# Optimization experiments

Hardware: AMD Instinct MI355X
Metric: run time of the kernel (lower is better)

Reference implementation:

```python
import jax, jax.numpy as jnp
import numpy as np
from jax import lax

B, CIN, COUT, H, W = 16, 320, 320, 64, 64
R, NUM_LORAS, LORA_STRIDE, SCALE, K = 4, 50, 4, 1.0, 3


def setup_inputs() -> dict:
    key = jax.random.key(0)
    k1, k2, k3, k4, k5, k6 = jax.random.split(key, 6)
    x = jax.random.normal(k1, (B, CIN, H, W), dtype=jnp.float32)
    lora_id = jax.random.randint(k2, (B,), 0, NUM_LORAS * LORA_STRIDE, dtype=jnp.int64)
    conv_w = jax.random.normal(k3, (COUT, CIN, K, K), dtype=jnp.float32) * (1.0 / np.sqrt(CIN * K * K))
    conv_b = jax.random.normal(k4, (COUT,), dtype=jnp.float32) * 0.01
    # stacked LoRA banks: down [L, r, Cin, 3, 3], up [L, Cout, r] (1x1 conv squeezed)
    down_w = jax.random.normal(k5, (NUM_LORAS, R, CIN, K, K), dtype=jnp.float32) * (1.0 / R)
    up_w = jax.random.normal(k6, (NUM_LORAS, COUT, R), dtype=jnp.float32) * 0.02
    return {"x": x, "conv_w": conv_w, "conv_b": conv_b, "down_w": down_w, "up_w": up_w, "lora_id": lora_id}


def _conv3x3(x, w):
    # x: [N, C, H, W], w: [O, C, 3, 3], stride 1, padding 1
    return lax.conv_general_dilated(x, w, (1, 1), [(1, 1), (1, 1)],
                                    dimension_numbers=("NCHW", "OIHW", "NCHW"))


def reference(x, conv_w, conv_b, down_w, up_w, lora_id):
    idx = lora_id // LORA_STRIDE                      # [B]
    active = (idx >= 0).astype(x.dtype)               # [B] mask; negative -> base conv only
    safe = jnp.clip(idx, 0, NUM_LORAS - 1)
    # base conv on full batch (dropout is identity at inference)
    base = _conv3x3(x, conv_w) + conv_b[None, :, None, None]  # [B, Cout, H, W]
    # per-sample gathered down conv (3x3), vmapped over batch (MoE-style dispatch)
    wd = down_w[safe]                                 # [B, r, Cin, 3, 3]
    down = jax.vmap(lambda xi, wi: _conv3x3(xi[None], wi)[0])(x, wd)  # [B, r, H, W]
    # per-sample 1x1 up conv as einsum with gathered up weights
    up = jnp.einsum("brhw,bor->bohw", down, up_w[safe])  # [B, Cout, H, W]
    return base + SCALE * up * active[:, None, None, None]
```

## Files before the change

### kernel.cpp

```cpp
#include <hip/hip_runtime.h>

typedef unsigned short ushort_t;
typedef unsigned int   uint_t;
typedef __attribute__((ext_vector_type(8))) short  short8;
typedef __attribute__((ext_vector_type(4))) float  float4v;
typedef __attribute__((ext_vector_type(4))) uint_t uint4v;
typedef __attribute__((ext_vector_type(2))) uint_t uint2v;

#define B_    16
#define CIN_  320
#define COUT_ 320
#define NLORA 50
#define R_    4
#define NCH   10

#define XCHUNK (66*66*32)
#define WCHUNK (9*COUT_*32)
#define XPAD_ELEMS ((size_t)B_ * NCH * XCHUNK)
#define WEFF_OFF   (XPAD_ELEMS * 2)

__device__ __forceinline__ ushort_t bf16rne(float f) {
  uint_t u = __float_as_uint(f);
  u = (u + 0x7FFFu + ((u >> 16) & 1u)) >> 16;
  return (ushort_t)u;
}

__device__ __forceinline__ void gld16(const ushort_t* g, ushort_t* l) {
  __builtin_amdgcn_global_load_lds(
      (const __attribute__((address_space(1))) void*)g,
      (__attribute__((address_space(3))) void*)l,
      16, 0, 0);
}

__global__ __launch_bounds__(256)
void pad_convert(const float* __restrict__ x, ushort_t* __restrict__ x_pad) {
  __shared__ float t[64][65];
  const int cc  = blockIdx.x;
  const int h   = blockIdx.y;
  const int b   = blockIdx.z;
  const int tid = threadIdx.x;
  #pragma unroll
  for (int it = 0; it < 4; ++it) {
    int idx = it * 256 + tid;
    int cl = idx >> 4, w4 = (idx & 15) * 4;
    float4v v = *(const float4v*)(x +
        (((size_t)(b * CIN_ + cc * 64 + cl)) * 64 + h) * 64 + w4);
    t[cl][w4] = v[0]; t[cl][w4 + 1] = v[1];
    t[cl][w4 + 2] = v[2]; t[cl][w4 + 3] = v[3];
  }
  __syncthreads();
  #pragma unroll
  for (int it = 0; it < 4; ++it) {
    int j  = it * 256 + tid;
    int cq = j & 15, wl = j >> 4;
    int cl = cq * 4;
    uint_t u0 = (uint_t)bf16rne(t[cl][wl])     | ((uint_t)bf16rne(t[cl + 1][wl]) << 16);
    uint_t u1 = (uint_t)bf16rne(t[cl + 2][wl]) | ((uint_t)bf16rne(t[cl + 3][wl]) << 16);
    int chunk = cc * 2 + (cl >> 5);
    uint2v u; u[0] = u0; u[1] = u1;
    *(uint2v*)(x_pad + (((size_t)(b * NCH + chunk) * 66 + (h + 1)) * 66 + (wl + 1)) * 32
               + (cl & 31)) = u;
  }
  if (h == 0) {
    #pragma unroll
    for (int s = 0; s < 2; ++s) {
      ushort_t* base = x_pad + (size_t)(b * NCH + cc * 2 + s) * XCHUNK;
      for (int g = tid; g < 528; g += 256) {
        int r = (g >= 264) ? 1 : 0;
        int g2 = g - r * 264;
        int col = g2 >> 2, qg = g2 & 3;
        *(uint4v*)(base + ((size_t)(r * 65) * 66 + col) * 32 + qg * 8) = (uint4v)0u;
      }
      for (int g = tid; g < 512; g += 256) {
        int row = 1 + (g >> 3);
        int col = ((g >> 2) & 1) * 65;
        int qg  = g & 3;
        *(uint4v*)(base + ((size_t)row * 66 + col) * 32 + qg * 8) = (uint4v)0u;
      }
    }
  }
}

__global__ __launch_bounds__(320)
void merge_weights(const float* __restrict__ conv_w, const float* __restrict__ down_w,
                   const float* __restrict__ up_w,  const void* __restrict__ lora,
                   ushort_t* __restrict__ W_eff) {
  const int o = blockIdx.x;
  const int b = blockIdx.y;
  const int tid = threadIdx.x;

  const int* p32 = (const int*)lora;
  bool odd0 = true;
  #pragma unroll
  for (int i = 1; i < 16; i += 2) odd0 = odd0 && (p32[i] == 0);
  long long raw = odd0 ? ((const long long*)lora)[b] : (long long)p32[b];
  long long idx = (raw >= 0) ? (raw >> 2) : -(((-raw) + 3) >> 2);
  float act = (idx >= 0) ? 1.0f : 0.0f;
  int l = (int)(idx < 0 ? 0 : (idx > (NLORA - 1) ? (NLORA - 1) : idx));

  float up[R_];
  #pragma unroll
  for (int r = 0; r < R_; ++r)
    up[r] = up_w[((size_t)l * COUT_ + o) * R_ + r] * act;

  const float* cw = conv_w + (size_t)o * (CIN_ * 9);
  const float* dw = down_w + (size_t)l * (R_ * CIN_ * 9);
  #pragma unroll
  for (int it = 0; it < 9; ++it) {
    int j = it * 320 + tid;
    float v = cw[j] + up[0] * dw[j] + up[1] * dw[2880 + j]
                    + up[2] * dw[5760 + j] + up[3] * dw[8640 + j];
    int c   = j / 9;
    int tap = j - c * 9;
    W_eff[(((size_t)(b * NCH + (c >> 5)) * 9 + tap) * COUT_ + o) * 32 + (c & 31)]
        = bf16rne(v);
  }
}

#define XG    1360
#define XGP   1408
#define WG    1152
#define TOTG  2560
#define BUF_B (TOTG * 16)

__global__ __launch_bounds__(512, 4)
void conv_main(const ushort_t* __restrict__ x_pad, const ushort_t* __restrict__ W_eff,
               const float* __restrict__ conv_b, float* __restrict__ out) {
  __shared__ __align__(16) char smem[2 * BUF_B];

  const int tid = threadIdx.x;
  const int lin = blockIdx.x;
  const int wg  = (lin & 7) * 320 + (lin >> 3);
  const int b   = wg / 160;
  const int rem = wg - b * 160;
  const int o0  = (rem >> 4) * 32;
  const int hw  = rem & 15;
  const int h0  = (hw & 7) * 8;
  const int w0  = (hw >> 3) * 32;

  const int wv = tid >> 6;
  const int la = tid & 15;
  const int q  = (tid >> 4) & 3;

  const ushort_t* psrc[5];
  int step[5];
  #pragma unroll
  for (int r = 0; r < 5; ++r) {
    int g = r * 512 + tid;
    if (g < XGP) {
      int gx = (g < XG) ? g : (XG - 1);
      int qq = gx & 3, t = gx >> 2;
      int hh = t / 34, ww = t - hh * 34;
      int sq = qq ^ ((ww >> 1) & 3);
      psrc[r] = x_pad + (size_t)b * NCH * XCHUNK
              + (((h0 + hh) * 66 + (w0 + ww)) * 32 + sq * 8);
      step[r] = XCHUNK;
    } else {
      int gw = g - XGP;
      int qq = gw & 3, t2 = gw >> 2;
      int o = t2 & 31, tap = t2 >> 5;
      int sq = qq ^ ((o >> 1) & 3);
      psrc[r] = W_eff + (size_t)b * NCH * WCHUNK
              + ((tap * COUT_ + o0 + o) * 32 + sq * 8);
      step[r] = WCHUNK;
    }
  }

  float4v acc[2][2];
  #pragma unroll
  for (int i = 0; i < 2; ++i)
    #pragma unroll
    for (int n = 0; n < 2; ++n) acc[i][n] = (float4v)0.0f;

  auto STAGE = [&](int sel) {
    ushort_t* bufb = (ushort_t*)(smem + sel * BUF_B);
    #pragma unroll
    for (int r = 0; r < 5; ++r) {
      gld16(psrc[r], bufb + (r * 512 + wv * 64) * 8);
      psrc[r] += step[r];
    }
  };

  STAGE(0);
  int cur = 0;
  for (int t = 0; t < NCH; ++t) {
    asm volatile("" ::: "memory");
    __builtin_amdgcn_s_barrier();
    asm volatile("" ::: "memory");
    if (t < NCH - 1) STAGE(cur ^ 1);
    __builtin_amdgcn_sched_barrier(0);
    if (t < NCH - 1) asm volatile("s_waitcnt vmcnt(5)" ::: "memory");
    else             asm volatile("s_waitcnt vmcnt(0)" ::: "memory");
    __builtin_amdgcn_sched_barrier(0);
    __builtin_amdgcn_s_barrier();
    asm volatile("" ::: "memory");

    const ushort_t* xb = (const ushort_t*)(smem + cur * BUF_B);
    const ushort_t* wb = xb + XGP * 8;
    #pragma unroll
    for (int tap = 0; tap < 9; ++tap) {
      const int kh = tap / 3, kw = tap - kh * 3;
      const int ob0 = la, ob1 = 16 + la;
      short8 bf0 = *(const short8*)(wb + ((tap * 32 + ob0) * 4 + (q ^ ((ob0 >> 1) & 3))) * 8);
      short8 bf1 = *(const short8*)(wb + ((tap * 32 + ob1) * 4 + (q ^ ((ob1 >> 1) & 3))) * 8);
      const int hh = wv + kh;
      #pragma unroll
      for (int i = 0; i < 2; ++i) {
        int ww = i * 16 + la + kw;
        short8 af = *(const short8*)(xb + ((hh * 34 + ww) * 4 + (q ^ ((ww >> 1) & 3))) * 8);
        acc[i][0] = __builtin_amdgcn_mfma_f32_16x16x32_bf16(af, bf0, acc[i][0], 0, 0, 0);
        acc[i][1] = __builtin_amdgcn_mfma_f32_16x16x32_bf16(af, bf1, acc[i][1], 0, 0, 0);
      }
    }
    cur ^= 1;
  }

  __syncthreads();
  float* lc = (float*)smem;
  #pragma unroll
  for (int n = 0; n < 2; ++n) {
    const int n_loc = n * 16 + la;
    #pragma unroll
    for (int i = 0; i < 2; ++i)
      *(float4v*)(lc + n_loc * 260 + wv * 32 + i * 16 + q * 4) = acc[i][n];
  }
  __syncthreads();
  const size_t ob = ((size_t)(b * COUT_ + o0)) * 4096 + h0 * 64 + w0;
  for (int f = tid; f < 32 * 64; f += 512) {
    int n_loc = f >> 6;
    int m4 = (f & 63) * 4;
    int row = m4 >> 5, col = m4 & 31;
    float4v v = *(const float4v*)(lc + n_loc * 260 + m4);
    v += conv_b[o0 + n_loc];
    *(float4v*)(out + ob + (size_t)n_loc * 4096 + row * 64 + col) = v;
  }
}

extern "C" void kernel_launch(void* const* d_in, const int* in_sizes, int n_in,
                              void* d_out, int out_size, void* d_ws, size_t ws_size,
                              hipStream_t stream) {
  const float* x      = (const float*)d_in[0];
  const float* conv_w = (const float*)d_in[1];
  const float* conv_b = (const float*)d_in[2];
  const float* down_w = (const float*)d_in[3];
  const float* up_w   = (const float*)d_in[4];
  const void*  lora   = d_in[5];
  float* out = (float*)d_out;

  ushort_t* x_pad = (ushort_t*)d_ws;
  ushort_t* W_eff = (ushort_t*)((char*)d_ws + WEFF_OFF);

  pad_convert  <<<dim3(5, 64, 16), 256, 0, stream>>>(x, x_pad);
  merge_weights<<<dim3(320, 16),   320, 0, stream>>>(conv_w, down_w, up_w, lora, W_eff);
  conv_main    <<<dim3(2560),      512, 0, stream>>>(x_pad, W_eff, conv_b, out);
}
```

Measured before the change: 303.2 us.

## Split LoRA into separate down-projection pass and fuse up-projection into conv epilogue

Stops merging the LoRA weights into a per-sample effective conv weight. The main conv now uses one shared bf16 base weight for all samples instead of per-batch W_eff. A separate small MFMA kernel computes the rank-4 down conv, and the up projection plus bias is applied in the conv epilogue, which writes directly from registers instead of staging through LDS. Shared weights improve cache reuse and avoid writing 16 copies of the merged weight, at the cost of two extra launches, a rank-16-padded down conv, and a different numeric path where the LoRA term is now computed in bf16 separately.

```diff
diff --git a/kernel.cpp b/kernel.cpp
--- a/kernel.cpp
+++ b/kernel.cpp
@@ -16,8 +16,11 @@
 
 #define XCHUNK (66*66*32)
 #define WCHUNK (9*COUT_*32)
-#define XPAD_ELEMS ((size_t)B_ * NCH * XCHUNK)
-#define WEFF_OFF   (XPAD_ELEMS * 2)
+#define DCHUNK (9*16*32)
+
+#define WB16_OFF  44605440ULL
+#define DWNE_OFF  46448640ULL
+#define DOWN_OFF  47923200ULL
 
 __device__ __forceinline__ ushort_t bf16rne(float f) {
   uint_t u = __float_as_uint(f);
@@ -30,6 +33,18 @@
       (const __attribute__((address_space(1))) void*)g,
       (__attribute__((address_space(3))) void*)l,
       16, 0, 0);
+}
+
+__device__ __forceinline__ void lora_idx(const void* lora, int b, int* l_out,
+                                         float* act_out) {
+  const int* p32 = (const int*)lora;
+  bool odd0 = true;
+  #pragma unroll
+  for (int i = 1; i < 16; i += 2) odd0 = odd0 && (p32[i] == 0);
+  long long raw = odd0 ? ((const long long*)lora)[b] : (long long)p32[b];
+  long long idx = (raw >= 0) ? (raw >> 2) : -(((-raw) + 3) >> 2);
+  *act_out = (idx >= 0) ? 1.0f : 0.0f;
+  *l_out = (int)(idx < 0 ? 0 : (idx > (NLORA - 1) ? (NLORA - 1) : idx));
 }
 
 __global__ __launch_bounds__(256)
@@ -81,39 +96,140 @@
   }
 }
 
-__global__ __launch_bounds__(320)
-void merge_weights(const float* __restrict__ conv_w, const float* __restrict__ down_w,
-                   const float* __restrict__ up_w,  const void* __restrict__ lora,
-                   ushort_t* __restrict__ W_eff) {
-  const int o = blockIdx.x;
-  const int b = blockIdx.y;
+__global__ __launch_bounds__(512)
+void wconv(const float* __restrict__ conv_w, ushort_t* __restrict__ wb16) {
+  int idx = blockIdx.x * 512 + threadIdx.x;
+  int c5 = idx & 31;
+  int o  = (idx >> 5) % COUT_;
+  int rest = idx / (COUT_ * 32);
+  int tap = rest % 9, chunk = rest / 9;
+  wb16[idx] = bf16rne(conv_w[((size_t)o * CIN_ + chunk * 32 + c5) * 9 + tap]);
+}
+
+__global__ __launch_bounds__(512)
+void dwnconv(const float* __restrict__ down_w, const void* __restrict__ lora,
+             ushort_t* __restrict__ dwn_eff) {
+  const int b = blockIdx.x;
+  int l; float act;
+  lora_idx(lora, b, &l, &act);
+  ushort_t* dst = dwn_eff + (size_t)b * (NCH * DCHUNK);
+  const float* src = down_w + (size_t)l * (R_ * CIN_ * 9);
+  for (int it = 0; it < 90; ++it) {
+    int idx = it * 512 + threadIdx.x;
+    int c5 = idx & 31;
+    int r  = (idx >> 5) & 15;
+    int rest = idx >> 9;
+    int tap = rest % 9, chunk = rest / 9;
+    float v = (r < R_) ? act * src[((size_t)(r * CIN_) + chunk * 32 + c5) * 9 + tap]
+                       : 0.0f;
+    dst[idx] = bf16rne(v);
+  }
+}
+
+#define LXG    1360
+#define LXGP   1408
+#define LWG    576
+#define LTOTG  2048
+#define LBUF_B (LTOTG * 16)
+
+__global__ __launch_bounds__(512)
+void lora_down(const ushort_t* __restrict__ x_pad, const ushort_t* __restrict__ dwn_eff,
+               float* __restrict__ down) {
+  __shared__ __align__(16) char smem[2 * LBUF_B];
+
   const int tid = threadIdx.x;
-
-  const int* p32 = (const int*)lora;
-  bool odd0 = true;
-  #pragma unroll
-  for (int i = 1; i < 16; i += 2) odd0 = odd0 && (p32[i] == 0);
-  long long raw = odd0 ? ((const long long*)lora)[b] : (long long)p32[b];
-  long long idx = (raw >= 0) ? (raw >> 2) : -(((-raw) + 3) >> 2);
-  float act = (idx >= 0) ? 1.0f : 0.0f;
-  int l = (int)(idx < 0 ? 0 : (idx > (NLORA - 1) ? (NLORA - 1) : idx));
-
-  float up[R_];
-  #pragma unroll
-  for (int r = 0; r < R_; ++r)
-    up[r] = up_w[((size_t)l * COUT_ + o) * R_ + r] * act;
-
-  const float* cw = conv_w + (size_t)o * (CIN_ * 9);
-  const float* dw = down_w + (size_t)l * (R_ * CIN_ * 9);
-  #pragma unroll
-  for (int it = 0; it < 9; ++it) {
-    int j = it * 320 + tid;
-    float v = cw[j] + up[0] * dw[j] + up[1] * dw[2880 + j]
-                    + up[2] * dw[5760 + j] + up[3] * dw[8640 + j];
-    int c   = j / 9;
-    int tap = j - c * 9;
-    W_eff[(((size_t)(b * NCH + (c >> 5)) * 9 + tap) * COUT_ + o) * 32 + (c & 31)]
-        = bf16rne(v);
+  const int lin = blockIdx.x;
+  const int b   = lin >> 4;
+  const int hw  = lin & 15;
+  const int h0  = (hw & 7) * 8;
+  const int w0  = (hw >> 3) * 32;
+
+  const int wv = tid >> 6;
+  const int la = tid & 15;
+  const int q  = (tid >> 4) & 3;
+
+  const ushort_t* psrc[4];
+  int step[4];
+  #pragma unroll
+  for (int r = 0; r < 4; ++r) {
+    int g = r * 512 + tid;
+    if (g < LXGP) {
+      int gx = (g < LXG) ? g : (LXG - 1);
+      int qq = gx & 3, t = gx >> 2;
+      int hh = t / 34, ww = t - hh * 34;
+      psrc[r] = x_pad + (size_t)b * NCH * XCHUNK
+              + (((h0 + hh) * 66 + (w0 + ww)) * 32 + (qq ^ ((ww >> 1) & 3)) * 8);
+      step[r] = XCHUNK;
+    } else {
+      int gw = g - LXGP;
+      if (gw > LWG - 1) gw = LWG - 1;
+      int qq = gw & 3, t2 = gw >> 2;
+      int rr = t2 & 15, tap = t2 >> 4;
+      psrc[r] = dwn_eff + (size_t)b * NCH * DCHUNK
+              + ((tap * 16 + rr) * 32 + (qq ^ ((rr >> 1) & 3)) * 8);
+      step[r] = DCHUNK;
+    }
+  }
+
+  const char* ax0[3]; const char* ax1[3];
+  #pragma unroll
+  for (int kw = 0; kw < 3; ++kw) {
+    int base = (wv * 34 + la + kw) * 64 + (q ^ (((la + kw) >> 1) & 3)) * 16;
+    ax0[kw] = smem + base;
+    ax1[kw] = smem + LBUF_B + base;
+  }
+  const int bfb = 22528 + la * 64 + (q ^ ((la >> 1) & 3)) * 16;
+  const char* aw0 = smem + bfb;
+  const char* aw1 = smem + LBUF_B + bfb;
+
+  float4v acc[2];
+  acc[0] = (float4v)0.0f; acc[1] = (float4v)0.0f;
+
+  auto STAGE = [&](int sel) {
+    ushort_t* bufb = (ushort_t*)(smem + sel * LBUF_B);
+    #pragma unroll
+    for (int r = 0; r < 4; ++r) {
+      gld16(psrc[r], bufb + (r * 512 + wv * 64) * 8);
+      psrc[r] += step[r];
+    }
+  };
+
+  auto PHASE = [&](const char* axA, const char* axB, const char* axC,
+                   const char* aw, bool do_stage, int sel_next) {
+    __builtin_amdgcn_s_barrier();
+    if (do_stage) STAGE(sel_next);
+    __builtin_amdgcn_sched_barrier(0);
+    if (do_stage) asm volatile("s_waitcnt vmcnt(4)" ::: "memory");
+    else          asm volatile("s_waitcnt vmcnt(0)" ::: "memory");
+    __builtin_amdgcn_sched_barrier(0);
+    __builtin_amdgcn_s_barrier();
+    __builtin_amdgcn_s_setprio(1);
+    #pragma unroll
+    for (int tap = 0; tap < 9; ++tap) {
+      const int kh = tap / 3, kw = tap - kh * 3;
+      const char* ax = (kw == 0) ? axA : ((kw == 1) ? axB : axC);
+      short8 bf = *(const short8*)(aw + tap * 1024);
+      #pragma unroll
+      for (int i = 0; i < 2; ++i) {
+        short8 af = *(const short8*)(ax + kh * 2176 + i * 1024);
+        acc[i] = __builtin_amdgcn_mfma_f32_16x16x32_bf16(af, bf, acc[i], 0, 0, 0);
+      }
+    }
+    __builtin_amdgcn_s_setprio(0);
+  };
+
+  STAGE(0);
+  #pragma unroll
+  for (int tp = 0; tp < 5; ++tp) {
+    PHASE(ax0[0], ax0[1], ax0[2], aw0, true,    1);
+    PHASE(ax1[0], ax1[1], ax1[2], aw1, tp < 4,  0);
+  }
+
+  if (la < R_) {
+    #pragma unroll
+    for (int i = 0; i < 2; ++i)
+      *(float4v*)(down + (((size_t)(b * R_ + la) * 64 + h0 + wv) * 64)
+                  + w0 + i * 16 + q * 4) = acc[i];
   }
 }
 
@@ -124,8 +240,10 @@
 #define BUF_B (TOTG * 16)
 
 __global__ __launch_bounds__(512, 4)
-void conv_main(const ushort_t* __restrict__ x_pad, const ushort_t* __restrict__ W_eff,
-               const float* __restrict__ conv_b, float* __restrict__ out) {
+void conv_main(const ushort_t* __restrict__ x_pad, const ushort_t* __restrict__ wb16,
+               const float* __restrict__ conv_b, const float* __restrict__ up_w,
+               const float* __restrict__ down, const void* __restrict__ lora,
+               float* __restrict__ out) {
   __shared__ __align__(16) char smem[2 * BUF_B];
 
   const int tid = threadIdx.x;
@@ -151,20 +269,28 @@
       int gx = (g < XG) ? g : (XG - 1);
       int qq = gx & 3, t = gx >> 2;
       int hh = t / 34, ww = t - hh * 34;
-      int sq = qq ^ ((ww >> 1) & 3);
       psrc[r] = x_pad + (size_t)b * NCH * XCHUNK
-              + (((h0 + hh) * 66 + (w0 + ww)) * 32 + sq * 8);
+              + (((h0 + hh) * 66 + (w0 + ww)) * 32 + (qq ^ ((ww >> 1) & 3)) * 8);
       step[r] = XCHUNK;
     } else {
       int gw = g - XGP;
       int qq = gw & 3, t2 = gw >> 2;
       int o = t2 & 31, tap = t2 >> 5;
-      int sq = qq ^ ((o >> 1) & 3);
-      psrc[r] = W_eff + (size_t)b * NCH * WCHUNK
-              + ((tap * COUT_ + o0 + o) * 32 + sq * 8);
+      psrc[r] = wb16 + ((size_t)(tap * COUT_ + o0 + o) * 32 + (qq ^ ((o >> 1) & 3)) * 8);
       step[r] = WCHUNK;
     }
   }
+
+  const char* ax0[3]; const char* ax1[3];
+  #pragma unroll
+  for (int kw = 0; kw < 3; ++kw) {
+    int base = (wv * 34 + la + kw) * 64 + (q ^ (((la + kw) >> 1) & 3)) * 16;
+    ax0[kw] = smem + base;
+    ax1[kw] = smem + BUF_B + base;
+  }
+  const int bfb = 22528 + la * 64 + (q ^ ((la >> 1) & 3)) * 16;
+  const char* aw0 = smem + bfb;
+  const char* aw1 = smem + BUF_B + bfb;
 
   float4v acc[2][2];
   #pragma unroll
@@ -181,58 +307,59 @@
     }
   };
 
-  STAGE(0);
-  int cur = 0;
-  for (int t = 0; t < NCH; ++t) {
-    asm volatile("" ::: "memory");
+  auto PHASE = [&](const char* axA, const char* axB, const char* axC,
+                   const char* aw, bool do_stage, int sel_next) {
     __builtin_amdgcn_s_barrier();
-    asm volatile("" ::: "memory");
-    if (t < NCH - 1) STAGE(cur ^ 1);
+    if (do_stage) STAGE(sel_next);
     __builtin_amdgcn_sched_barrier(0);
-    if (t < NCH - 1) asm volatile("s_waitcnt vmcnt(5)" ::: "memory");
-    else             asm volatile("s_waitcnt vmcnt(0)" ::: "memory");
+    if (do_stage) asm volatile("s_waitcnt vmcnt(5)" ::: "memory");
+    else          asm volatile("s_waitcnt vmcnt(0)" ::: "memory");
     __builtin_amdgcn_sched_barrier(0);
     __builtin_amdgcn_s_barrier();
-    asm volatile("" ::: "memory");
-
-    const ushort_t* xb = (const ushort_t*)(smem + cur * BUF_B);
-    const ushort_t* wb = xb + XGP * 8;
+    __builtin_amdgcn_s_setprio(1);
     #pragma unroll
     for (int tap = 0; tap < 9; ++tap) {
       const int kh = tap / 3, kw = tap - kh * 3;
-      const int ob0 = la, ob1 = 16 + la;
-      short8 bf0 = *(const short8*)(wb + ((tap * 32 + ob0) * 4 + (q ^ ((ob0 >> 1) & 3))) * 8);
-      short8 bf1 = *(const short8*)(wb + ((tap * 32 + ob1) * 4 + (q ^ ((ob1 >> 1) & 3))) * 8);
-      const int hh = wv + kh;
+      const char* ax = (kw == 0) ? axA : ((kw == 1) ? axB : axC);
+      short8 bf0 = *(const short8*)(aw + tap * 2048);
+      short8 bf1 = *(const short8*)(aw + tap * 2048 + 1024);
       #pragma unroll
       for (int i = 0; i < 2; ++i) {
-        int ww = i * 16 + la + kw;
-        short8 af = *(const short8*)(xb + ((hh * 34 + ww) * 4 + (q ^ ((ww >> 1) & 3))) * 8);
+        short8 af = *(const short8*)(ax + kh * 2176 + i * 1024);
         acc[i][0] = __builtin_amdgcn_mfma_f32_16x16x32_bf16(af, bf0, acc[i][0], 0, 0, 0);
         acc[i][1] = __builtin_amdgcn_mfma_f32_16x16x32_bf16(af, bf1, acc[i][1], 0, 0, 0);
       }
     }
-    cur ^= 1;
-  }
-
-  __syncthreads();
-  float* lc = (float*)smem;
-  #pragma unroll
-  for (int n = 0; n < 2; ++n) {
-    const int n_loc = n * 16 + la;
-    #pragma unroll
-    for (int i = 0; i < 2; ++i)
-      *(float4v*)(lc + n_loc * 260 + wv * 32 + i * 16 + q * 4) = acc[i][n];
-  }
-  __syncthreads();
-  const size_t ob = ((size_t)(b * COUT_ + o0)) * 4096 + h0 * 64 + w0;
-  for (int f = tid; f < 32 * 64; f += 512) {
-    int n_loc = f >> 6;
-    int m4 = (f & 63) * 4;
-    int row = m4 >> 5, col = m4 & 31;
-    float4v v = *(const float4v*)(lc + n_loc * 260 + m4);
-    v += conv_b[o0 + n_loc];
-    *(float4v*)(out + ob + (size_t)n_loc * 4096 + row * 64 + col) = v;
+    __builtin_amdgcn_s_setprio(0);
+  };
+
+  STAGE(0);
+  #pragma unroll
+  for (int tp = 0; tp < 5; ++tp) {
+    PHASE(ax0[0], ax0[1], ax0[2], aw0, true,   1);
+    PHASE(ax1[0], ax1[1], ax1[2], aw1, tp < 4, 0);
+  }
+
+  int l; float act;
+  lora_idx(lora, b, &l, &act);
+  const float* upb = up_w + (size_t)l * (COUT_ * R_);
+  #pragma unroll
+  for (int i = 0; i < 2; ++i) {
+    float4v d[4];
+    #pragma unroll
+    for (int r = 0; r < 4; ++r)
+      d[r] = *(const float4v*)(down + (((size_t)(b * R_ + r) * 64 + h0 + wv) * 64)
+                               + w0 + i * 16 + q * 4);
+    #pragma unroll
+    for (int n = 0; n < 2; ++n) {
+      const int o = o0 + n * 16 + la;
+      float4v u = *(const float4v*)(upb + o * R_);
+      float4v v = acc[i][n];
+      v += conv_b[o];
+      v += u[0] * d[0] + u[1] * d[1] + u[2] * d[2] + u[3] * d[3];
+      *(float4v*)(out + (((size_t)(b * COUT_ + o) * 64 + h0 + wv) * 64)
+                  + w0 + i * 16 + q * 4) = v;
+    }
   }
 }
 
@@ -247,10 +374,15 @@
   const void*  lora   = d_in[5];
   float* out = (float*)d_out;
 
-  ushort_t* x_pad = (ushort_t*)d_ws;
-  ushort_t* W_eff = (ushort_t*)((char*)d_ws + WEFF_OFF);
-
-  pad_convert  <<<dim3(5, 64, 16), 256, 0, stream>>>(x, x_pad);
-  merge_weights<<<dim3(320, 16),   320, 0, stream>>>(conv_w, down_w, up_w, lora, W_eff);
-  conv_main    <<<dim3(2560),      512, 0, stream>>>(x_pad, W_eff, conv_b, out);
-}
+  ushort_t* x_pad   = (ushort_t*)d_ws;
+  ushort_t* wb16    = (ushort_t*)((char*)d_ws + WB16_OFF);
+  ushort_t* dwn_eff = (ushort_t*)((char*)d_ws + DWNE_OFF);
+  float*    down    = (float*)((char*)d_ws + DOWN_OFF);
+
+  pad_convert<<<dim3(5, 64, 16), 256, 0, stream>>>(x, x_pad);
+  wconv      <<<dim3(1800),      512, 0, stream>>>(conv_w, wb16);
+  dwnconv    <<<dim3(16),        512, 0, stream>>>(down_w, lora, dwn_eff);
+  lora_down  <<<dim3(256),       512, 0, stream>>>(x_pad, dwn_eff, down);
+  conv_main  <<<dim3(2560),      512, 0, stream>>>(x_pad, wb16, conv_b, up_w,
+                                                   down, lora, out);
+}
```

New measurement: 302.0 us. No clear change (-0.4%).
